# Kernel tuning notes

Hardware: AMD Instinct MI355X
Metric: run time of the kernel (lower is better)

## Reference

```python
import jax, jax.numpy as jnp
import numpy as np

D_IN = 768
D_OUT = 768
N_HEADS = 12
HEAD_DIM = D_OUT // N_HEADS


def setup_inputs() -> dict:
    key = jax.random.key(0)
    ks = jax.random.split(key, 6)
    B, S = 2, 4096
    x = jax.random.normal(ks[0], (B, S, D_IN), dtype=jnp.float32)
    s = 0.02
    Wq = jax.random.normal(ks[1], (D_IN, D_OUT), dtype=jnp.float32) * s
    Wk = jax.random.normal(ks[2], (D_IN, D_OUT), dtype=jnp.float32) * s
    Wv = jax.random.normal(ks[3], (D_IN, D_OUT), dtype=jnp.float32) * s
    Wo = jax.random.normal(ks[4], (D_OUT, D_OUT), dtype=jnp.float32) * s
    bo = jnp.zeros((D_OUT,), dtype=jnp.float32)
    return {"x": x, "Wq": Wq, "Wk": Wk, "Wv": Wv, "Wo": Wo, "bo": bo}


def reference(x, Wq, Wk, Wv, Wo, bo):
    B, S, _ = x.shape
    # QKV projections (no bias), reshape to [B, H, S, Dh]
    q = (x @ Wq).reshape(B, S, N_HEADS, HEAD_DIM).transpose(0, 2, 1, 3)
    k = (x @ Wk).reshape(B, S, N_HEADS, HEAD_DIM).transpose(0, 2, 1, 3)
    v = (x @ Wv).reshape(B, S, N_HEADS, HEAD_DIM).transpose(0, 2, 1, 3)
    # scores: [B, H, S, S], causal mask, scaled softmax
    scores = jnp.einsum('bhqd,bhkd->bhqk', q, k)
    causal = jnp.triu(jnp.ones((S, S), dtype=bool), k=1)
    scores = jnp.where(causal, -jnp.inf, scores)
    attn = jax.nn.softmax(scores / np.sqrt(HEAD_DIM).astype(np.float32), axis=-1)
    # dropout p=0.0 -> identity
    ctx = jnp.einsum('bhqk,bhkd->bqhd', attn, v).reshape(B, S, D_OUT)
    return ctx @ Wo + bo
```

## Files before the change

### kernel.cpp

```cpp
#include <hip/hip_runtime.h>

#define S 4096
#define BATCH 2
#define D 768
#define NH 12
#define DH 64
#define NROWS (BATCH * S)
#define N_ITEMS (32 * NH * BATCH)
#define CTR_OFF 67633152

typedef __attribute__((ext_vector_type(8))) short bf16x8;
typedef __attribute__((ext_vector_type(4))) float f32x4;

__device__ __forceinline__ unsigned short f2bf(float f) {
    unsigned u = __builtin_bit_cast(unsigned, f);
    u += 0x7fff + ((u >> 16) & 1);
    return (unsigned short)(u >> 16);
}

__device__ __forceinline__ float fexp2(float x) {
#if __has_builtin(__builtin_amdgcn_exp2f)
    return __builtin_amdgcn_exp2f(x);
#else
    return exp2f(x);
#endif
}

#define GLDS16(g, l)                                                   \
    __builtin_amdgcn_global_load_lds(                                  \
        (const __attribute__((address_space(1))) void*)(g),            \
        (__attribute__((address_space(3))) void*)(l), 16, 0, 0)

__global__ __launch_bounds__(256) void cvt_x(const float* __restrict__ x,
                                             unsigned short* __restrict__ xb)
{
    int i = (blockIdx.x * 256 + threadIdx.x) * 4;
    float4 v = *(const float4*)(x + i);
    ushort4 o = make_ushort4(f2bf(v.x), f2bf(v.y), f2bf(v.z), f2bf(v.w));
    *(ushort4*)(xb + i) = o;
}

__global__ __launch_bounds__(256) void cvt_w(
    const float* __restrict__ Wq, const float* __restrict__ Wk,
    const float* __restrict__ Wv, const float* __restrict__ Wo,
    unsigned short* __restrict__ wt)
{
    __shared__ float tile[32][33];
    const int z = blockIdx.z;
    const float* W = (z == 0) ? Wq : (z == 1) ? Wk : (z == 2) ? Wv : Wo;
    const int k0 = blockIdx.x * 32, n0 = blockIdx.y * 32;
    const int t = threadIdx.x;
    const int r = t >> 3, c4 = (t & 7) * 4;

    float4 v = *(const float4*)(W + (size_t)(k0 + r) * D + n0 + c4);
    tile[r][c4 + 0] = v.x; tile[r][c4 + 1] = v.y;
    tile[r][c4 + 2] = v.z; tile[r][c4 + 3] = v.w;
    __syncthreads();
    ushort4 o = make_ushort4(f2bf(tile[c4 + 0][r]), f2bf(tile[c4 + 1][r]),
                             f2bf(tile[c4 + 2][r]), f2bf(tile[c4 + 3][r]));
    *(ushort4*)(wt + ((size_t)z * D + n0 + r) * D + k0 + c4) = o;
}

__global__ __launch_bounds__(256) void gemm_qkv(
    const unsigned short* __restrict__ xb,
    const unsigned short* __restrict__ wt,
    unsigned short* __restrict__ qb, unsigned short* __restrict__ kb,
    unsigned short* __restrict__ vtb)
{
    __shared__ unsigned short As[128 * 64];
    __shared__ unsigned short Bs[128 * 64];

    const int t = threadIdx.x;
    const int lane = t & 63, w = t >> 6;
    const int l16 = lane & 15, quad = lane >> 4;
    const int wm = w & 1, wn = w >> 1;
    const int m0 = blockIdx.x * 128;
    const int n0g = blockIdx.y * 128;
    const int z = n0g / 768;
    const int c0 = n0g - z * 768;
    const unsigned short* Wz = wt + (size_t)z * D * D;

    f32x4 acc[4][4] = {};

    for (int k0 = 0; k0 < D; k0 += 64) {
#pragma unroll
        for (int i = 0; i < 4; ++i) {
            int g = i * 256 + w * 64 + lane;
            int row = g >> 3, cl = g & 7, cg = cl ^ (row & 7);
            GLDS16(xb + (size_t)(m0 + row) * D + k0 + cg * 8,
                   As + (size_t)(i * 256 + w * 64) * 8);
            GLDS16(Wz + (size_t)(c0 + row) * D + k0 + cg * 8,
                   Bs + (size_t)(i * 256 + w * 64) * 8);
        }
        __syncthreads();
#pragma unroll
        for (int kk = 0; kk < 2; ++kk) {
            bf16x8 af[4], bf_[4];
#pragma unroll
            for (int mt = 0; mt < 4; ++mt) {
                int r = wm * 64 + mt * 16 + l16;
                int c = kk * 4 + quad;
                af[mt] = *(const bf16x8*)&As[(r * 8 + (c ^ (r & 7))) * 8];
            }
#pragma unroll
            for (int nt = 0; nt < 4; ++nt) {
                int r = wn * 64 + nt * 16 + l16;
                int c = kk * 4 + quad;
                bf_[nt] = *(const bf16x8*)&Bs[(r * 8 + (c ^ (r & 7))) * 8];
            }
#pragma unroll
            for (int mt = 0; mt < 4; ++mt)
#pragma unroll
                for (int nt = 0; nt < 4; ++nt)
                    acc[mt][nt] = __builtin_amdgcn_mfma_f32_16x16x32_bf16(
                        af[mt], bf_[nt], acc[mt][nt], 0, 0, 0);
        }
        __syncthreads();
    }

    if (z < 2) {
        unsigned short* outp = (z == 0) ? qb : kb;
        const float scale = (z == 0) ? 0.18033688011112042f : 1.0f;
#pragma unroll
        for (int mt = 0; mt < 4; ++mt) {
#pragma unroll
            for (int reg = 0; reg < 4; ++reg) {
                int m = wm * 64 + mt * 16 + quad * 4 + reg;
                int ng = m0 + m;
                int b = ng >> 12, s = ng & 4095;
#pragma unroll
                for (int nt = 0; nt < 4; ++nt) {
                    int n = c0 + wn * 64 + nt * 16 + l16;
                    int h = n >> 6, dh = n & 63;
                    outp[(((size_t)b * NH + h) * S + s) * DH + dh] =
                        f2bf(acc[mt][nt][reg] * scale);
                }
            }
        }
    } else {
#pragma unroll
        for (int mt = 0; mt < 4; ++mt) {
#pragma unroll
            for (int nt = 0; nt < 4; ++nt) {
                int m = wm * 64 + mt * 16 + quad * 4;
                int ng = m0 + m;
                int b = ng >> 12, s = ng & 4095;
                int n = c0 + wn * 64 + nt * 16 + l16;
                int h = n >> 6, dh = n & 63;
                ushort4 p = make_ushort4(
                    f2bf(acc[mt][nt][0]), f2bf(acc[mt][nt][1]),
                    f2bf(acc[mt][nt][2]), f2bf(acc[mt][nt][3]));
                *(ushort4*)(vtb + (((size_t)b * NH + h) * DH + dh) * S + s) = p;
            }
        }
    }
}

__global__ __launch_bounds__(256) void attn_mfma(
    const unsigned short* __restrict__ qg,
    const unsigned short* __restrict__ kg,
    const unsigned short* __restrict__ vtg,
    unsigned short* __restrict__ ctxb,
    int* __restrict__ work_ctr)
{
    __shared__ unsigned short Ks[2][64 * 64];
    __shared__ unsigned short Vs[2][64 * 64];
    __shared__ unsigned short Ps[4][32][64];
    __shared__ int s_item;

    const float INF = __builtin_inff();
    const int t = threadIdx.x;
    const int w = t >> 6, lane = t & 63;
    const int l16 = lane & 15, quad = lane >> 4;
    const int a7 = l16 & 7;
    const int sg = w * 64 + lane;

    for (;;) {
        if (t == 0) s_item = atomicAdd(work_ctr, 1);
        __syncthreads();
        const int p = s_item;
        if (p >= N_ITEMS) return;

        const int qt = 31 - (p / (NH * BATCH));
        const int hb = p % (NH * BATCH);
        const int h = hb % NH, b = hb / NH;
        const size_t hbase = ((size_t)b * NH + h) * (size_t)S * DH;
        const unsigned short* kp = kg + hbase;
        const unsigned short* vp = vtg + hbase;

        bf16x8 bq[2][2];
#pragma unroll
        for (int qs = 0; qs < 2; ++qs) {
            int qrow = qt * 128 + w * 32 + qs * 16 + l16;
#pragma unroll
            for (int kk = 0; kk < 2; ++kk)
                bq[qs][kk] = *(const bf16x8*)(qg + hbase + (size_t)qrow * DH +
                                              kk * 32 + quad * 8);
        }

        f32x4 acc_o[2][4] = {};
        float lsum[2] = {0.f, 0.f};

        const int jmax = 2 * qt + 1, jd = 2 * qt;

#pragma unroll
        for (int i = 0; i < 2; ++i) {
            int g = i * 256 + sg;
            int row = g >> 3, cl = g & 7, cg = cl ^ (row & 7);
            GLDS16(kp + (size_t)row * DH + cg * 8,
                   &Ks[0][(size_t)(i * 256 + w * 64) * 8]);
            GLDS16(vp + (size_t)row * S + cg * 8,
                   &Vs[0][(size_t)(i * 256 + w * 64) * 8]);
        }

        for (int j = 0; j <= jmax; ++j) {
            const int cur = j & 1;
            __syncthreads();
            if (j < jmax) {
#pragma unroll
                for (int i = 0; i < 2; ++i) {
                    int g = i * 256 + sg;
                    int row = g >> 3, cl = g & 7, cg = cl ^ (row & 7);
                    GLDS16(kp + (size_t)((j + 1) * 64 + row) * DH + cg * 8,
                           &Ks[cur ^ 1][(size_t)(i * 256 + w * 64) * 8]);
                    GLDS16(vp + (size_t)row * S + (j + 1) * 64 + cg * 8,
                           &Vs[cur ^ 1][(size_t)(i * 256 + w * 64) * 8]);
                }
            }

            const unsigned short* Kc = Ks[cur];
            const unsigned short* Vc = Vs[cur];

            f32x4 acc_s[2][4] = {};
#pragma unroll
            for (int kk = 0; kk < 2; ++kk)
#pragma unroll
                for (int ms = 0; ms < 4; ++ms) {
                    int r = ms * 16 + l16, c = kk * 4 + quad;
                    bf16x8 ak = *(const bf16x8*)&Kc[(r * 8 + (c ^ a7)) * 8];
#pragma unroll
                    for (int qs = 0; qs < 2; ++qs)
                        acc_s[qs][ms] = __builtin_amdgcn_mfma_f32_16x16x32_bf16(
                            ak, bq[qs][kk], acc_s[qs][ms], 0, 0, 0);
                }

            if (j >= jd) {
#pragma unroll
                for (int qs = 0; qs < 2; ++qs) {
                    int qrow_g = qt * 128 + w * 32 + qs * 16 + l16;
#pragma unroll
                    for (int ms = 0; ms < 4; ++ms)
#pragma unroll
                        for (int reg = 0; reg < 4; ++reg)
                            if ((j * 64 + ms * 16 + quad * 4 + reg) > qrow_g)
                                acc_s[qs][ms][reg] = -INF;
                }
            }

#pragma unroll
            for (int qs = 0; qs < 2; ++qs) {
#pragma unroll
                for (int ms = 0; ms < 4; ++ms) {
                    float e0 = fexp2(acc_s[qs][ms][0]);
                    float e1 = fexp2(acc_s[qs][ms][1]);
                    float e2 = fexp2(acc_s[qs][ms][2]);
                    float e3 = fexp2(acc_s[qs][ms][3]);
                    lsum[qs] += (e0 + e1) + (e2 + e3);
                    unsigned u01 = __builtin_amdgcn_perm(
                        __builtin_bit_cast(unsigned, e1),
                        __builtin_bit_cast(unsigned, e0), 0x07060302u);
                    unsigned u23 = __builtin_amdgcn_perm(
                        __builtin_bit_cast(unsigned, e3),
                        __builtin_bit_cast(unsigned, e2), 0x07060302u);
                    int c8 = ms * 2 + (quad >> 1);
                    *(uint2*)&Ps[w][qs * 16 + l16]
                               [(c8 ^ a7) * 8 + (quad & 1) * 4] =
                        make_uint2(u01, u23);
                }
            }

#pragma unroll
            for (int kk = 0; kk < 2; ++kk) {
                bf16x8 bp[2];
#pragma unroll
                for (int qs = 0; qs < 2; ++qs)
                    bp[qs] = *(const bf16x8*)&Ps[w][qs * 16 + l16]
                                                [((kk * 4 + quad) ^ a7) * 8];
#pragma unroll
                for (int d = 0; d < 4; ++d) {
                    int r = d * 16 + l16, c = kk * 4 + quad;
                    bf16x8 av = *(const bf16x8*)&Vc[(r * 8 + (c ^ a7)) * 8];
#pragma unroll
                    for (int qs = 0; qs < 2; ++qs)
                        acc_o[qs][d] = __builtin_amdgcn_mfma_f32_16x16x32_bf16(
                            av, bp[qs], acc_o[qs][d], 0, 0, 0);
                }
            }
        }

#pragma unroll
        for (int qs = 0; qs < 2; ++qs) {
            float tot = lsum[qs];
            tot += __shfl_xor(tot, 16);
            tot += __shfl_xor(tot, 32);
            float inv = 1.f / tot;
            lsum[qs] = 0.f;
            int qrow = qt * 128 + w * 32 + qs * 16 + l16;
            size_t base = ((size_t)(b * S + qrow)) * D + h * 64;
#pragma unroll
            for (int d = 0; d < 4; ++d) {
                ushort4 o;
                o.x = f2bf(acc_o[qs][d][0] * inv);
                o.y = f2bf(acc_o[qs][d][1] * inv);
                o.z = f2bf(acc_o[qs][d][2] * inv);
                o.w = f2bf(acc_o[qs][d][3] * inv);
                *(ushort4*)(ctxb + base + d * 16 + quad * 4) = o;
            }
        }
    }
}

__global__ __launch_bounds__(256) void gemm_out(
    const unsigned short* __restrict__ ctxb,
    const unsigned short* __restrict__ wt,
    const float* __restrict__ bo,
    float* __restrict__ out)
{
    __shared__ unsigned short As[128 * 64];
    __shared__ unsigned short Bs[128 * 64];

    const int t = threadIdx.x;
    const int lane = t & 63, w = t >> 6;
    const int l16 = lane & 15, quad = lane >> 4;
    const int wm = w & 1, wn = w >> 1;
    const int m0 = blockIdx.x * 128;
    const int n0 = blockIdx.y * 128;
    const unsigned short* Wz = wt + (size_t)3 * D * D;

    f32x4 acc[4][4] = {};

    for (int k0 = 0; k0 < D; k0 += 64) {
#pragma unroll
        for (int i = 0; i < 4; ++i) {
            int g = i * 256 + w * 64 + lane;
            int row = g >> 3, cl = g & 7, cg = cl ^ (row & 7);
            GLDS16(ctxb + (size_t)(m0 + row) * D + k0 + cg * 8,
                   As + (size_t)(i * 256 + w * 64) * 8);
            GLDS16(Wz + (size_t)(n0 + row) * D + k0 + cg * 8,
                   Bs + (size_t)(i * 256 + w * 64) * 8);
        }
        __syncthreads();
#pragma unroll
        for (int kk = 0; kk < 2; ++kk) {
            bf16x8 af[4], bf_[4];
#pragma unroll
            for (int mt = 0; mt < 4; ++mt) {
                int r = wm * 64 + mt * 16 + l16;
                int c = kk * 4 + quad;
                af[mt] = *(const bf16x8*)&As[(r * 8 + (c ^ (r & 7))) * 8];
            }
#pragma unroll
            for (int nt = 0; nt < 4; ++nt) {
                int r = wn * 64 + nt * 16 + l16;
                int c = kk * 4 + quad;
                bf_[nt] = *(const bf16x8*)&Bs[(r * 8 + (c ^ (r & 7))) * 8];
            }
#pragma unroll
            for (int mt = 0; mt < 4; ++mt)
#pragma unroll
                for (int nt = 0; nt < 4; ++nt)
                    acc[mt][nt] = __builtin_amdgcn_mfma_f32_16x16x32_bf16(
                        af[mt], bf_[nt], acc[mt][nt], 0, 0, 0);
        }
        __syncthreads();
    }

    float bv[4];
#pragma unroll
    for (int nt = 0; nt < 4; ++nt)
        bv[nt] = bo[n0 + wn * 64 + nt * 16 + l16];
#pragma unroll
    for (int mt = 0; mt < 4; ++mt)
#pragma unroll
        for (int reg = 0; reg < 4; ++reg) {
            int m = m0 + wm * 64 + mt * 16 + quad * 4 + reg;
#pragma unroll
            for (int nt = 0; nt < 4; ++nt)
                out[(size_t)m * D + n0 + wn * 64 + nt * 16 + l16] =
                    acc[mt][nt][reg] + bv[nt];
        }
}

extern "C" void kernel_launch(void* const* d_in, const int* in_sizes, int n_in,
                              void* d_out, int out_size, void* d_ws, size_t ws_size,
                              hipStream_t stream)
{
    const float* x  = (const float*)d_in[0];
    const float* Wq = (const float*)d_in[1];
    const float* Wk = (const float*)d_in[2];
    const float* Wv = (const float*)d_in[3];
    const float* Wo = (const float*)d_in[4];
    const float* bo = (const float*)d_in[5];
    float* out = (float*)d_out;

    const size_t elems = (size_t)NROWS * D;
    unsigned short* xb   = (unsigned short*)d_ws;
    unsigned short* wt   = xb + elems;
    unsigned short* q    = wt + (size_t)4 * D * D;
    unsigned short* k    = q + elems;
    unsigned short* vt   = k + elems;
    unsigned short* ctxb = vt + elems;
    int* work_ctr = (int*)((char*)d_ws + CTR_OFF);

    hipMemsetAsync(work_ctr, 0, sizeof(int), stream);

    cvt_x<<<NROWS * D / 1024, 256, 0, stream>>>(x, xb);
    dim3 gw(D / 32, D / 32, 4);
    cvt_w<<<gw, 256, 0, stream>>>(Wq, Wk, Wv, Wo, wt);

    dim3 g1(NROWS / 128, (3 * D) / 128);
    gemm_qkv<<<g1, 256, 0, stream>>>(xb, wt, q, k, vt);

    attn_mfma<<<640, 256, 0, stream>>>(q, k, vt, ctxb, work_ctr);

    dim3 g3(NROWS / 128, D / 128);
    gemm_out<<<g3, 256, 0, stream>>>(ctxb, wt, bo, out);
}
```

Before: 258.3 us.

## Drop K/V double buffering in attention to cut LDS and raise occupancy

Replaces the double-buffered K/V shared-memory tiles with single buffers, loading each tile and then synchronizing before compute, with an extra barrier after compute. This halves LDS use for K/V so more blocks fit per CU, and the grid is raised from 640 to 1024 persistent blocks to use that occupancy. It gives up the overlap of the next tile's global loads with the current tile's compute and adds barriers, relying on other resident blocks to hide the latency instead.

```diff
diff --git a/kernel.cpp b/kernel.cpp
--- a/kernel.cpp
+++ b/kernel.cpp
@@ -163,8 +163,8 @@
     unsigned short* __restrict__ ctxb,
     int* __restrict__ work_ctr)
 {
-    __shared__ unsigned short Ks[2][64 * 64];
-    __shared__ unsigned short Vs[2][64 * 64];
+    __shared__ unsigned short Ks[64 * 64];
+    __shared__ unsigned short Vs[64 * 64];
     __shared__ unsigned short Ps[4][32][64];
     __shared__ int s_item;
 
@@ -176,6 +176,7 @@
     const int sg = w * 64 + lane;
 
     for (;;) {
+        __syncthreads();
         if (t == 0) s_item = atomicAdd(work_ctr, 1);
         __syncthreads();
         const int p = s_item;
@@ -203,33 +204,17 @@
 
         const int jmax = 2 * qt + 1, jd = 2 * qt;
 
-#pragma unroll
-        for (int i = 0; i < 2; ++i) {
-            int g = i * 256 + sg;
-            int row = g >> 3, cl = g & 7, cg = cl ^ (row & 7);
-            GLDS16(kp + (size_t)row * DH + cg * 8,
-                   &Ks[0][(size_t)(i * 256 + w * 64) * 8]);
-            GLDS16(vp + (size_t)row * S + cg * 8,
-                   &Vs[0][(size_t)(i * 256 + w * 64) * 8]);
-        }
-
         for (int j = 0; j <= jmax; ++j) {
-            const int cur = j & 1;
+#pragma unroll
+            for (int i = 0; i < 2; ++i) {
+                int g = i * 256 + sg;
+                int row = g >> 3, cl = g & 7, cg = cl ^ (row & 7);
+                GLDS16(kp + (size_t)(j * 64 + row) * DH + cg * 8,
+                       &Ks[(size_t)(i * 256 + w * 64) * 8]);
+                GLDS16(vp + (size_t)row * S + j * 64 + cg * 8,
+                       &Vs[(size_t)(i * 256 + w * 64) * 8]);
+            }
             __syncthreads();
-            if (j < jmax) {
-#pragma unroll
-                for (int i = 0; i < 2; ++i) {
-                    int g = i * 256 + sg;
-                    int row = g >> 3, cl = g & 7, cg = cl ^ (row & 7);
-                    GLDS16(kp + (size_t)((j + 1) * 64 + row) * DH + cg * 8,
-                           &Ks[cur ^ 1][(size_t)(i * 256 + w * 64) * 8]);
-                    GLDS16(vp + (size_t)row * S + (j + 1) * 64 + cg * 8,
-                           &Vs[cur ^ 1][(size_t)(i * 256 + w * 64) * 8]);
-                }
-            }
-
-            const unsigned short* Kc = Ks[cur];
-            const unsigned short* Vc = Vs[cur];
 
             f32x4 acc_s[2][4] = {};
 #pragma unroll
@@ -237,7 +222,7 @@
 #pragma unroll
                 for (int ms = 0; ms < 4; ++ms) {
                     int r = ms * 16 + l16, c = kk * 4 + quad;
-                    bf16x8 ak = *(const bf16x8*)&Kc[(r * 8 + (c ^ a7)) * 8];
+                    bf16x8 ak = *(const bf16x8*)&Ks[(r * 8 + (c ^ a7)) * 8];
 #pragma unroll
                     for (int qs = 0; qs < 2; ++qs)
                         acc_s[qs][ms] = __builtin_amdgcn_mfma_f32_16x16x32_bf16(
@@ -289,13 +274,14 @@
 #pragma unroll
                 for (int d = 0; d < 4; ++d) {
                     int r = d * 16 + l16, c = kk * 4 + quad;
-                    bf16x8 av = *(const bf16x8*)&Vc[(r * 8 + (c ^ a7)) * 8];
+                    bf16x8 av = *(const bf16x8*)&Vs[(r * 8 + (c ^ a7)) * 8];
 #pragma unroll
                     for (int qs = 0; qs < 2; ++qs)
                         acc_o[qs][d] = __builtin_amdgcn_mfma_f32_16x16x32_bf16(
                             av, bp[qs], acc_o[qs][d], 0, 0, 0);
                 }
             }
+            __syncthreads();
         }
 
 #pragma unroll
@@ -304,7 +290,6 @@
             tot += __shfl_xor(tot, 16);
             tot += __shfl_xor(tot, 32);
             float inv = 1.f / tot;
-            lsum[qs] = 0.f;
             int qrow = qt * 128 + w * 32 + qs * 16 + l16;
             size_t base = ((size_t)(b * S + qrow)) * D + h * 64;
 #pragma unroll
@@ -421,7 +406,7 @@
     dim3 g1(NROWS / 128, (3 * D) / 128);
     gemm_qkv<<<g1, 256, 0, stream>>>(xb, wt, q, k, vt);
 
-    attn_mfma<<<640, 256, 0, stream>>>(q, k, vt, ctxb, work_ctr);
+    attn_mfma<<<1024, 256, 0, stream>>>(q, k, vt, ctxb, work_ctr);
 
     dim3 g3(NROWS / 128, D / 128);
     gemm_out<<<g3, 256, 0, stream>>>(ctxb, wt, bo, out);
```

Result: slower. 265.2 us (+2.7%).
